# Kernel optimization log

Hardware: AMD Instinct MI355X
Metric: run time of the kernel (lower is better)

Reference implementation:

```python
import jax, jax.numpy as jnp
import numpy as np

SHAPES = ((96, 144), (48, 72), (24, 36), (12, 18))
BS, EMBED = 2, 256
HEADS, LEVELS, POINTS = 8, 4, 4
NEMBED = EMBED // HEADS
LEN_V = sum(h * w for h, w in SHAPES)
LEN_Q = LEN_V  # encoder self-attention: every pixel is a query


def _pos_grid_init():
    # Faithful re-implementation of MultiScaleDeformableAttention.pos_grid_init
    thetas = jnp.arange(HEADS, dtype=jnp.float32) * (2.0 * np.pi / HEADS)
    g = jnp.stack([jnp.cos(thetas), jnp.sin(thetas)], -1)
    g = g / jnp.max(jnp.abs(g), axis=-1, keepdims=True)
    g = jnp.tile(g.reshape(HEADS, 1, 1, 2), (1, LEVELS, POINTS, 1))
    scale = (jnp.arange(POINTS, dtype=jnp.float32) + 1.0)[None, None, :, None]
    return g * scale  # [HEADS, LEVELS, POINTS, 2]


def setup_inputs() -> dict:
    ks = jax.random.split(jax.random.key(0), 7)
    return {
        'query': jax.random.normal(ks[0], (BS, LEN_Q, EMBED), jnp.float32),
        'ref_points': jax.random.uniform(ks[1], (BS, LEN_Q, LEVELS, 2), jnp.float32),
        'value': jax.random.normal(ks[2], (BS, LEN_V, EMBED), jnp.float32),
        'pad_mask': jnp.ones((BS, LEN_V), dtype=bool),
        'value_proj_kernel': jax.random.normal(ks[3], (EMBED, HEADS, NEMBED), jnp.float32) * 0.05,
        'value_proj_bias': jnp.zeros((HEADS, NEMBED), jnp.float32),
        'sampling_offsets_kernel': jax.random.normal(ks[4], (EMBED, HEADS, LEVELS, POINTS, 2), jnp.float32) * 0.01,
        'sampling_offsets_bias': _pos_grid_init(),
        'attn_kernel': jax.random.normal(ks[5], (EMBED, HEADS, LEVELS * POINTS), jnp.float32) * 0.02,
        'attn_bias': jnp.zeros((HEADS, LEVELS * POINTS), jnp.float32),
        'out_kernel': jax.random.normal(ks[6], (HEADS, NEMBED, EMBED), jnp.float32) * 0.05,
        'out_bias': jnp.zeros((EMBED,), jnp.float32),
        'train': 0,
    }


def _bilinear(im, grid, w, h):
    """Batched 2D bilinear interpolation, zero outside the image.

    im:   [B, h*w, e] flattened feature map
    grid: [B, N, 2] normalized coords (pixel centers at (x+0.5)/w, (y+0.5)/h)
    Returns [B, N, e]. Identical math to the original gather-based kernel:
    out-of-bounds corner weights are zeroed, so zero-padding the image by 1
    reproduces the 'empty'-pad + masked-weight scheme exactly.
    """
    B, _, e = im.shape
    imp = jnp.pad(im.reshape(B, h, w, e), ((0, 0), (1, 1), (1, 1), (0, 0)))
    imp = imp.reshape(B, (h + 2) * (w + 2), e)
    x = grid[..., 0] * w - 0.5
    y = grid[..., 1] * h - 0.5
    x0 = jnp.floor(x).astype(jnp.int32)
    y0 = jnp.floor(y).astype(jnp.int32)
    x1 = x0 + 1
    y1 = y0 + 1

    def gather(yy, xx):
        idx = jnp.clip(yy + 1, 0, h + 1) * (w + 2) + jnp.clip(xx + 1, 0, w + 1)
        return jnp.take_along_axis(imp, idx[..., None], axis=1)  # [B, N, e]

    x0f, y0f = x0.astype(x.dtype), y0.astype(y.dtype)
    x1f, y1f = x1.astype(x.dtype), y1.astype(y.dtype)
    inx0 = (x0 >= 0) & (x0 <= w - 1)
    inx1 = (x1 >= 0) & (x1 <= w - 1)
    iny0 = (y0 >= 0) & (y0 <= h - 1)
    iny1 = (y1 >= 0) & (y1 <= h - 1)
    wa = jnp.where(inx0 & iny0, (x1f - x) * (y1f - y), 0.0)
    wb = jnp.where(inx0 & iny1, (x1f - x) * (y - y0f), 0.0)
    wc = jnp.where(inx1 & iny0, (x - x0f) * (y1f - y), 0.0)
    wd = jnp.where(inx1 & iny1, (x - x0f) * (y - y0f), 0.0)
    return (gather(y0, x0) * wa[..., None] + gather(y1, x0) * wb[..., None]
            + gather(y0, x1) * wc[..., None] + gather(y1, x1) * wd[..., None])


def _forward(query, ref_points, value, pad_mask, vpk, vpb, sok, sob, ak, ab, okern, obias):
    bs, len_q, _ = query.shape
    len_v = value.shape[1]
    # value projection + pad masking -> [bs*H, len_v, nembed]
    v = jnp.einsum('bve,ehd->bvhd', value, vpk) + vpb
    v = jnp.where(pad_mask[..., None, None], v, 0)
    v = v.transpose(0, 2, 1, 3).reshape(bs * HEADS, len_v, NEMBED)
    # sampling locations (ref_dim == 2 branch) -> [bs*H, L, P*len_q, 2]
    off = jnp.einsum('bqe,ehlpc->bqhlpc', query, sok) + sob
    offset_norm = jnp.array([[w, h] for h, w in SHAPES], dtype=query.dtype)  # [L, 2]
    loc = ref_points[:, :, None, :, None, :] + off / offset_norm[None, None, None, :, None, :]
    loc = loc.transpose(0, 2, 3, 4, 1, 5).reshape(bs * HEADS, LEVELS, POINTS * len_q, 2)
    # attention weights (softmax over L*P) -> [bs*H, len_q, L*P]
    aw = jnp.einsum('bqe,ehm->bqhm', query, ak) + ab
    aw = jax.nn.softmax(aw, axis=-1)
    aw = aw.transpose(0, 2, 1, 3).reshape(bs * HEADS, len_q, LEVELS * POINTS)
    # per-level bilinear sampling, concatenated level-major over (level, point)
    starts = np.cumsum([0] + [h * w for h, w in SHAPES])
    sampled = []
    for li, (h, w) in enumerate(SHAPES):
        vl = v[:, starts[li]:starts[li + 1], :]
        s = _bilinear(vl, loc[:, li], w, h)  # [bs*H, P*len_q, nembed]
        sampled.append(s.reshape(bs * HEADS, POINTS, len_q, NEMBED))
    sampled = jnp.concatenate(sampled, axis=1)  # [bs*H, L*P, len_q, nembed]
    x = jnp.einsum('blqe,bql->bqe', sampled, aw)
    x = x.reshape(bs, HEADS, len_q, NEMBED)
    # output projection: DenseGeneral over (heads, nembed)
    return jnp.einsum('bhqe,hed->bqd', x, okern) + obias


def reference(query, ref_points, value, pad_mask, value_proj_kernel, value_proj_bias,
              sampling_offsets_kernel, sampling_offsets_bias, attn_kernel, attn_bias,
              out_kernel, out_bias, train):
    del train  # eval mode (no remat); math is identical
    return _forward(query, ref_points, value, pad_mask, value_proj_kernel, value_proj_bias,
                    sampling_offsets_kernel, sampling_offsets_bias, attn_kernel, attn_bias,
                    out_kernel, out_bias)
```

## Files before the change

### kernel.cpp

```cpp
#include <hip/hip_runtime.h>
#include <math.h>

#define LEN 18360
#define M_ROWS (2 * LEN)
#define NTASK (16 * LEN)

typedef unsigned short u16;
typedef __attribute__((ext_vector_type(8))) short bf16x8;
typedef __attribute__((ext_vector_type(4))) float f32x4;

__device__ __forceinline__ u16 f2bf(float f) {
  unsigned u = __float_as_uint(f);
  return (u16)((u + 0x7fffu + ((u >> 16) & 1u)) >> 16);
}
__device__ __forceinline__ void async_cp16(const void* g, void* l) {
  __builtin_amdgcn_global_load_lds(
      (const __attribute__((address_space(1))) unsigned*)g,
      (__attribute__((address_space(3))) unsigned*)l, 16, 0, 0);
}

template <int OUT>
__global__ __launch_bounds__(256) void gemm_mfma_k(
    const u16* __restrict__ A, const u16* __restrict__ Bt,
    const float* __restrict__ bias, void* __restrict__ Cv, int M, int N) {
  __shared__ u16 A_lds[8 * 512];
  __shared__ u16 B_lds[8 * 512];

  const int tid = threadIdx.x;
  const int w = tid >> 6;
  const int lane = tid & 63;
  const int wm = w & 1, wn = w >> 1;
  const int m0 = (int)blockIdx.y << 7;
  const int n0 = (int)blockIdx.x << 7;

  const int mr = lane & 15;
  const int kq = (lane >> 4) * 8;

  f32x4 acc[4][4];
#pragma unroll
  for (int i = 0; i < 4; i++)
#pragma unroll
    for (int j = 0; j < 4; j++) acc[i][j] = (f32x4){0.f, 0.f, 0.f, 0.f};

  for (int k0 = 0; k0 < 256; k0 += 32) {
    __syncthreads();
#pragma unroll
    for (int t = 0; t < 2; t++) {
      const int st = 2 * w + t;
      const int ga = min(m0 + st * 16 + mr, M - 1);
      async_cp16(A + (size_t)ga * 256 + k0 + kq, &A_lds[st * 512]);
      const int gb = n0 + st * 16 + mr;
      async_cp16(Bt + (size_t)gb * 256 + k0 + kq, &B_lds[st * 512]);
    }
    __syncthreads();

    bf16x8 af[4], bf[4];
#pragma unroll
    for (int i = 0; i < 4; i++)
      af[i] = *(const bf16x8*)&A_lds[(wm * 4 + i) * 512 + lane * 8];
#pragma unroll
    for (int j = 0; j < 4; j++)
      bf[j] = *(const bf16x8*)&B_lds[(wn * 4 + j) * 512 + lane * 8];
#pragma unroll
    for (int i = 0; i < 4; i++)
#pragma unroll
      for (int j = 0; j < 4; j++)
        acc[i][j] = __builtin_amdgcn_mfma_f32_16x16x32_bf16(bf[j], af[i],
                                                            acc[i][j], 0, 0, 0);
  }

#pragma unroll
  for (int i = 0; i < 4; i++) {
    const int row = m0 + wm * 64 + i * 16 + mr;
    if (row >= M) continue;
#pragma unroll
    for (int j = 0; j < 4; j++) {
      const int col = n0 + wn * 64 + j * 16 + (lane >> 4) * 4;
      const float4 b4 = *(const float4*)(bias + col);
      float4 o;
      o.x = acc[i][j][0] + b4.x;
      o.y = acc[i][j][1] + b4.y;
      o.z = acc[i][j][2] + b4.z;
      o.w = acc[i][j][3] + b4.w;
      if (OUT == 0) {
        *(float4*)((float*)Cv + (size_t)row * N + col) = o;
      } else if (OUT == 1) {
        const int b = row >= LEN;
        const int lv = row - b * LEN;
        const int h = col >> 5, d = col & 31;
        *(float4*)((float*)Cv + ((size_t)((b * 8 + h) * LEN + lv)) * 32 + d) = o;
      } else {
        uint2 p;
        p.x = (unsigned)f2bf(o.x) | ((unsigned)f2bf(o.y) << 16);
        p.y = (unsigned)f2bf(o.z) | ((unsigned)f2bf(o.w) << 16);
        *(uint2*)((u16*)Cv + (size_t)row * N + col) = p;
      }
    }
  }
}

__global__ __launch_bounds__(256) void cast_qv_k(const float* __restrict__ q,
                                                 const float* __restrict__ v,
                                                 u16* __restrict__ qb,
                                                 u16* __restrict__ vb) {
  const size_t i = ((size_t)blockIdx.x * 256 + threadIdx.x) * 4;
  float4 a = *(const float4*)(q + i);
  uint2 p;
  p.x = (unsigned)f2bf(a.x) | ((unsigned)f2bf(a.y) << 16);
  p.y = (unsigned)f2bf(a.z) | ((unsigned)f2bf(a.w) << 16);
  *(uint2*)&qb[i] = p;
  float4 c = *(const float4*)(v + i);
  p.x = (unsigned)f2bf(c.x) | ((unsigned)f2bf(c.y) << 16);
  p.y = (unsigned)f2bf(c.z) | ((unsigned)f2bf(c.w) << 16);
  *(uint2*)&vb[i] = p;
}

__global__ __launch_bounds__(256) void wcast_k(
    const float* __restrict__ vpk, const float* __restrict__ sok,
    const float* __restrict__ ak, const float* __restrict__ ok,
    u16* __restrict__ vpk_t, u16* __restrict__ sok_t, u16* __restrict__ ak_t,
    u16* __restrict__ ok_t) {
  const int gid = blockIdx.x * 256 + threadIdx.x;
  if (gid < 65536) {
    const int d = gid, n = d >> 8, k = d & 255;
    vpk_t[d] = f2bf(vpk[k * 256 + n]);
  } else if (gid < 131072) {
    const int d = gid - 65536, n = d >> 8, k = d & 255;
    sok_t[d] = f2bf(sok[k * 256 + n]);
  } else if (gid < 163840) {
    const int d = gid - 131072, n = d >> 8, k = d & 255;
    ak_t[d] = f2bf(ak[k * 128 + n]);
  } else {
    const int d = gid - 163840, n = d >> 8, k = d & 255;
    ok_t[d] = f2bf(ok[k * 256 + n]);
  }
}

__global__ __launch_bounds__(256) void sampler_k(
    const float* __restrict__ v,
    const u16* __restrict__ offb,
    const u16* __restrict__ awb,
    const float* __restrict__ refp,
    u16* __restrict__ xb)
{
  __shared__ int2 meta[4][258];
  const int tid = threadIdx.x;

  const int cW[4] = {144, 72, 36, 18};
  const int cH[4] = {96, 48, 24, 12};
  const int cS[4] = {0, 13824, 17280, 18144};

  {
    const int t = tid >> 4;
    const int s = tid & 15;
    const int l = s >> 2;

    const int task = (blockIdx.x << 4) + t;
    const int q = task % LEN;
    const int bh = task / LEN;
    const int h = bh & 7;
    const int b = bh >> 3;
    const size_t qrow = (size_t)(b * LEN + q);

    const float logit =
        __uint_as_float((unsigned)awb[qrow * 128 + h * 16 + s] << 16);
    float mx = logit;
#pragma unroll
    for (int m = 1; m < 16; m <<= 1) mx = fmaxf(mx, __shfl_xor(mx, m, 16));
    const float e = __expf(logit - mx);
    float ssum = e;
#pragma unroll
    for (int m = 1; m < 16; m <<= 1) ssum += __shfl_xor(ssum, m, 16);
    const float wsm = e / ssum;

    const int W = cW[l], H = cH[l], ST = cS[l];
    const float2 rp = ((const float2*)(refp + qrow * 8))[l];
    const unsigned upair = ((const unsigned*)(offb + qrow * 256 + h * 32))[s];
    const float ox = __uint_as_float(upair << 16);
    const float oy = __uint_as_float(upair & 0xffff0000u);
    const float X = rp.x * (float)W + ox - 0.5f;
    const float Y = rp.y * (float)H + oy - 0.5f;
    const float fx = floorf(X), fy = floorf(Y);
    const int x0 = (int)fx, y0 = (int)fy;
    const float dx = X - fx, dy = Y - fy;
    const float ux = 1.f - dx, uy = 1.f - dy;
    const bool bx0 = (unsigned)x0 < (unsigned)W;
    const bool bx1 = (unsigned)(x0 + 1) < (unsigned)W;
    const bool by0 = (unsigned)y0 < (unsigned)H;
    const bool by1 = (unsigned)(y0 + 1) < (unsigned)H;
    const int xc0 = min(max(x0, 0), W - 1);
    const int xc1 = min(max(x0 + 1, 0), W - 1);
    const int yc0 = min(max(y0, 0), H - 1);
    const int yc1 = min(max(y0 + 1, 0), H - 1);
    const float w00 = (bx0 & by0) ? wsm * ux * uy : 0.f;
    const float w10 = (bx1 & by0) ? wsm * dx * uy : 0.f;
    const float w01 = (bx0 & by1) ? wsm * ux * dy : 0.f;
    const float w11 = (bx1 & by1) ? wsm * dx * dy : 0.f;

    meta[0][tid] = make_int2((ST + yc0 * W + xc0) << 7, __float_as_int(w00));
    meta[1][tid] = make_int2((ST + yc0 * W + xc1) << 7, __float_as_int(w10));
    meta[2][tid] = make_int2((ST + yc1 * W + xc0) << 7, __float_as_int(w01));
    meta[3][tid] = make_int2((ST + yc1 * W + xc1) << 7, __float_as_int(w11));
  }
  __syncthreads();

  const int u = tid >> 5;
  const int lane = tid & 31;
  const int c = lane >> 3;
  const int dq = lane & 7;

#pragma unroll
  for (int rep = 0; rep < 2; rep++) {
    const int t = u + rep * 8;
    const int task = (blockIdx.x << 4) + t;
    const int q = task % LEN;
    const int bh = task / LEN;
    const int h = bh & 7;
    const int b = bh >> 3;
    const size_t qrow = (size_t)(b * LEN + q);
    const char* vb = (const char*)v + (size_t)bh * LEN * 128;

    float4 acc = make_float4(0.f, 0.f, 0.f, 0.f);
#pragma unroll
    for (int s = 0; s < 16; s++) {
      const int2 m2 = meta[c][t * 16 + s];
      const float wgt = __int_as_float(m2.y);
      const float4 vv =
          *(const float4*)(vb + (size_t)(unsigned)m2.x + (dq << 4));
      acc.x = fmaf(wgt, vv.x, acc.x);
      acc.y = fmaf(wgt, vv.y, acc.y);
      acc.z = fmaf(wgt, vv.z, acc.z);
      acc.w = fmaf(wgt, vv.w, acc.w);
    }
#pragma unroll
    for (int m = 8; m <= 16; m <<= 1) {
      acc.x += __shfl_xor(acc.x, m, 32);
      acc.y += __shfl_xor(acc.y, m, 32);
      acc.z += __shfl_xor(acc.z, m, 32);
      acc.w += __shfl_xor(acc.w, m, 32);
    }
    if (c == 0) {
      uint2 p;
      p.x = (unsigned)f2bf(acc.x) | ((unsigned)f2bf(acc.y) << 16);
      p.y = (unsigned)f2bf(acc.z) | ((unsigned)f2bf(acc.w) << 16);
      *(uint2*)&xb[qrow * 256 + h * 32 + (dq << 2)] = p;
    }
  }
}

extern "C" void kernel_launch(void* const* d_in, const int* in_sizes, int n_in,
                              void* d_out, int out_size, void* d_ws,
                              size_t ws_size, hipStream_t stream) {
  (void)in_sizes; (void)n_in; (void)out_size; (void)ws_size;

  const float* query = (const float*)d_in[0];
  const float* refp = (const float*)d_in[1];
  const float* value = (const float*)d_in[2];
  const float* vpk = (const float*)d_in[4];
  const float* vpb = (const float*)d_in[5];
  const float* sok = (const float*)d_in[6];
  const float* sob = (const float*)d_in[7];
  const float* ak = (const float*)d_in[8];
  const float* ab = (const float*)d_in[9];
  const float* okern = (const float*)d_in[10];
  const float* obias = (const float*)d_in[11];

  char* ws = (char*)d_ws;
  float* v_ws = (float*)ws;
  char* p = ws + (size_t)M_ROWS * 256 * 4;
  u16* off_b = (u16*)p; p += (size_t)M_ROWS * 256 * 2;
  u16* aw_b = (u16*)p;  p += (size_t)M_ROWS * 128 * 2;
  u16* qbf = (u16*)p;   p += (size_t)M_ROWS * 256 * 2;
  u16* vbf = (u16*)p;   p += (size_t)M_ROWS * 256 * 2;
  u16* vpk_t = (u16*)p; p += 65536 * 2;
  u16* sok_t = (u16*)p; p += 65536 * 2;
  u16* ak_t = (u16*)p;  p += 32768 * 2;
  u16* ok_t = (u16*)p;
  u16* x_b = qbf;

  const dim3 blk(256);
  const int mtiles = (M_ROWS + 127) / 128;

  cast_qv_k<<<dim3(2350080 / 256), blk, 0, stream>>>(query, value, qbf, vbf);
  wcast_k<<<dim3(896), blk, 0, stream>>>(vpk, sok, ak, okern, vpk_t, sok_t,
                                         ak_t, ok_t);
  gemm_mfma_k<1><<<dim3(2, mtiles), blk, 0, stream>>>(vbf, vpk_t, vpb, v_ws,
                                                      M_ROWS, 256);
  gemm_mfma_k<2><<<dim3(2, mtiles), blk, 0, stream>>>(qbf, sok_t, sob, off_b,
                                                      M_ROWS, 256);
  gemm_mfma_k<2><<<dim3(1, mtiles), blk, 0, stream>>>(qbf, ak_t, ab, aw_b,
                                                      M_ROWS, 128);
  sampler_k<<<dim3(NTASK / 16), blk, 0, stream>>>(v_ws, off_b, aw_b, refp,
                                                  x_b);
  gemm_mfma_k<0><<<dim3(2, mtiles), blk, 0, stream>>>(x_b, ok_t, obias,
                                                      (float*)d_out, M_ROWS,
                                                      256);
}
```

Before: 299.3 us.

## Merge projection GEMMs into one launch and store projected values as bf16

After: 275.5 us. 1.09x faster.

```diff
diff --git a/kernel.cpp b/kernel.cpp
--- a/kernel.cpp
+++ b/kernel.cpp
@@ -19,20 +19,34 @@
       (__attribute__((address_space(3))) unsigned*)l, 16, 0, 0);
 }
 
-template <int OUT>
 __global__ __launch_bounds__(256) void gemm_mfma_k(
-    const u16* __restrict__ A, const u16* __restrict__ Bt,
-    const float* __restrict__ bias, void* __restrict__ Cv, int M, int N) {
+    const u16* __restrict__ A0, const u16* __restrict__ Bt0,
+    const float* __restrict__ bias0, void* __restrict__ C0, int N0, int nt0,
+    int mode0, int split, const u16* __restrict__ A1,
+    const u16* __restrict__ Bt1, const float* __restrict__ bias1,
+    void* __restrict__ C1, int N1, int nt1, int mode1) {
   __shared__ u16 A_lds[8 * 512];
   __shared__ u16 B_lds[8 * 512];
+
+  int bid = (int)blockIdx.x;
+  const u16* A;
+  const u16* Bt;
+  const float* bias;
+  void* Cv;
+  int N, nt, mode;
+  if (bid < split) {
+    A = A0; Bt = Bt0; bias = bias0; Cv = C0; N = N0; nt = nt0; mode = mode0;
+  } else {
+    bid -= split;
+    A = A1; Bt = Bt1; bias = bias1; Cv = C1; N = N1; nt = nt1; mode = mode1;
+  }
+  const int n0 = (bid % nt) << 7;
+  const int m0 = (bid / nt) << 7;
 
   const int tid = threadIdx.x;
   const int w = tid >> 6;
   const int lane = tid & 63;
   const int wm = w & 1, wn = w >> 1;
-  const int m0 = (int)blockIdx.y << 7;
-  const int n0 = (int)blockIdx.x << 7;
-
   const int mr = lane & 15;
   const int kq = (lane >> 4) * 8;
 
@@ -47,7 +61,7 @@
 #pragma unroll
     for (int t = 0; t < 2; t++) {
       const int st = 2 * w + t;
-      const int ga = min(m0 + st * 16 + mr, M - 1);
+      const int ga = min(m0 + st * 16 + mr, M_ROWS - 1);
       async_cp16(A + (size_t)ga * 256 + k0 + kq, &A_lds[st * 512]);
       const int gb = n0 + st * 16 + mr;
       async_cp16(Bt + (size_t)gb * 256 + k0 + kq, &B_lds[st * 512]);
@@ -72,7 +86,7 @@
 #pragma unroll
   for (int i = 0; i < 4; i++) {
     const int row = m0 + wm * 64 + i * 16 + mr;
-    if (row >= M) continue;
+    if (row >= M_ROWS) continue;
 #pragma unroll
     for (int j = 0; j < 4; j++) {
       const int col = n0 + wn * 64 + j * 16 + (lane >> 4) * 4;
@@ -82,13 +96,16 @@
       o.y = acc[i][j][1] + b4.y;
       o.z = acc[i][j][2] + b4.z;
       o.w = acc[i][j][3] + b4.w;
-      if (OUT == 0) {
+      if (mode == 0) {
         *(float4*)((float*)Cv + (size_t)row * N + col) = o;
-      } else if (OUT == 1) {
+      } else if (mode == 1) {
         const int b = row >= LEN;
         const int lv = row - b * LEN;
         const int h = col >> 5, d = col & 31;
-        *(float4*)((float*)Cv + ((size_t)((b * 8 + h) * LEN + lv)) * 32 + d) = o;
+        uint2 p;
+        p.x = (unsigned)f2bf(o.x) | ((unsigned)f2bf(o.y) << 16);
+        p.y = (unsigned)f2bf(o.z) | ((unsigned)f2bf(o.w) << 16);
+        *(uint2*)((u16*)Cv + ((size_t)((b * 8 + h) * LEN + lv)) * 32 + d) = p;
       } else {
         uint2 p;
         p.x = (unsigned)f2bf(o.x) | ((unsigned)f2bf(o.y) << 16);
@@ -118,28 +135,31 @@
 __global__ __launch_bounds__(256) void wcast_k(
     const float* __restrict__ vpk, const float* __restrict__ sok,
     const float* __restrict__ ak, const float* __restrict__ ok,
-    u16* __restrict__ vpk_t, u16* __restrict__ sok_t, u16* __restrict__ ak_t,
-    u16* __restrict__ ok_t) {
+    const float* __restrict__ sob, const float* __restrict__ ab,
+    u16* __restrict__ vpk_t, u16* __restrict__ sa_t, u16* __restrict__ ok_t,
+    float* __restrict__ bias_cat) {
   const int gid = blockIdx.x * 256 + threadIdx.x;
   if (gid < 65536) {
     const int d = gid, n = d >> 8, k = d & 255;
     vpk_t[d] = f2bf(vpk[k * 256 + n]);
   } else if (gid < 131072) {
     const int d = gid - 65536, n = d >> 8, k = d & 255;
-    sok_t[d] = f2bf(sok[k * 256 + n]);
+    sa_t[d] = f2bf(sok[k * 256 + n]);
   } else if (gid < 163840) {
     const int d = gid - 131072, n = d >> 8, k = d & 255;
-    ak_t[d] = f2bf(ak[k * 128 + n]);
-  } else {
+    sa_t[65536 + d] = f2bf(ak[k * 128 + n]);
+  } else if (gid < 229376) {
     const int d = gid - 163840, n = d >> 8, k = d & 255;
     ok_t[d] = f2bf(ok[k * 256 + n]);
+  } else if (gid < 229760) {
+    const int d = gid - 229376;
+    bias_cat[d] = (d < 256) ? sob[d] : ab[d - 256];
   }
 }
 
 __global__ __launch_bounds__(256) void sampler_k(
-    const float* __restrict__ v,
-    const u16* __restrict__ offb,
-    const u16* __restrict__ awb,
+    const u16* __restrict__ v,
+    const u16* __restrict__ offaw,
     const float* __restrict__ refp,
     u16* __restrict__ xb)
 {
@@ -161,9 +181,9 @@
     const int h = bh & 7;
     const int b = bh >> 3;
     const size_t qrow = (size_t)(b * LEN + q);
-
-    const float logit =
-        __uint_as_float((unsigned)awb[qrow * 128 + h * 16 + s] << 16);
+    const u16* rowp = offaw + qrow * 384;
+
+    const float logit = __uint_as_float((unsigned)rowp[256 + h * 16 + s] << 16);
     float mx = logit;
 #pragma unroll
     for (int m = 1; m < 16; m <<= 1) mx = fmaxf(mx, __shfl_xor(mx, m, 16));
@@ -175,7 +195,7 @@
 
     const int W = cW[l], H = cH[l], ST = cS[l];
     const float2 rp = ((const float2*)(refp + qrow * 8))[l];
-    const unsigned upair = ((const unsigned*)(offb + qrow * 256 + h * 32))[s];
+    const unsigned upair = ((const unsigned*)(rowp + h * 32))[s];
     const float ox = __uint_as_float(upair << 16);
     const float oy = __uint_as_float(upair & 0xffff0000u);
     const float X = rp.x * (float)W + ox - 0.5f;
@@ -197,10 +217,10 @@
     const float w01 = (bx0 & by1) ? wsm * ux * dy : 0.f;
     const float w11 = (bx1 & by1) ? wsm * dx * dy : 0.f;
 
-    meta[0][tid] = make_int2((ST + yc0 * W + xc0) << 7, __float_as_int(w00));
-    meta[1][tid] = make_int2((ST + yc0 * W + xc1) << 7, __float_as_int(w10));
-    meta[2][tid] = make_int2((ST + yc1 * W + xc0) << 7, __float_as_int(w01));
-    meta[3][tid] = make_int2((ST + yc1 * W + xc1) << 7, __float_as_int(w11));
+    meta[0][tid] = make_int2((ST + yc0 * W + xc0) << 6, __float_as_int(w00));
+    meta[1][tid] = make_int2((ST + yc0 * W + xc1) << 6, __float_as_int(w10));
+    meta[2][tid] = make_int2((ST + yc1 * W + xc0) << 6, __float_as_int(w01));
+    meta[3][tid] = make_int2((ST + yc1 * W + xc1) << 6, __float_as_int(w11));
   }
   __syncthreads();
 
@@ -218,19 +238,18 @@
     const int h = bh & 7;
     const int b = bh >> 3;
     const size_t qrow = (size_t)(b * LEN + q);
-    const char* vb = (const char*)v + (size_t)bh * LEN * 128;
+    const char* vb = (const char*)v + (size_t)bh * LEN * 64;
 
     float4 acc = make_float4(0.f, 0.f, 0.f, 0.f);
 #pragma unroll
     for (int s = 0; s < 16; s++) {
       const int2 m2 = meta[c][t * 16 + s];
       const float wgt = __int_as_float(m2.y);
-      const float4 vv =
-          *(const float4*)(vb + (size_t)(unsigned)m2.x + (dq << 4));
-      acc.x = fmaf(wgt, vv.x, acc.x);
-      acc.y = fmaf(wgt, vv.y, acc.y);
-      acc.z = fmaf(wgt, vv.z, acc.z);
-      acc.w = fmaf(wgt, vv.w, acc.w);
+      const uint2 pv = *(const uint2*)(vb + (size_t)(unsigned)m2.x + (dq << 3));
+      acc.x = fmaf(wgt, __uint_as_float(pv.x << 16), acc.x);
+      acc.y = fmaf(wgt, __uint_as_float(pv.x & 0xffff0000u), acc.y);
+      acc.z = fmaf(wgt, __uint_as_float(pv.y << 16), acc.z);
+      acc.w = fmaf(wgt, __uint_as_float(pv.y & 0xffff0000u), acc.w);
     }
 #pragma unroll
     for (int m = 8; m <= 16; m <<= 1) {
@@ -265,34 +284,28 @@
   const float* okern = (const float*)d_in[10];
   const float* obias = (const float*)d_in[11];
 
-  char* ws = (char*)d_ws;
-  float* v_ws = (float*)ws;
-  char* p = ws + (size_t)M_ROWS * 256 * 4;
-  u16* off_b = (u16*)p; p += (size_t)M_ROWS * 256 * 2;
-  u16* aw_b = (u16*)p;  p += (size_t)M_ROWS * 128 * 2;
-  u16* qbf = (u16*)p;   p += (size_t)M_ROWS * 256 * 2;
-  u16* vbf = (u16*)p;   p += (size_t)M_ROWS * 256 * 2;
-  u16* vpk_t = (u16*)p; p += 65536 * 2;
-  u16* sok_t = (u16*)p; p += 65536 * 2;
-  u16* ak_t = (u16*)p;  p += 32768 * 2;
-  u16* ok_t = (u16*)p;
+  char* p = (char*)d_ws;
+  u16* v_ws = (u16*)p;   p += (size_t)M_ROWS * 256 * 2;
+  u16* offaw = (u16*)p;  p += (size_t)M_ROWS * 384 * 2;
+  u16* qbf = (u16*)p;    p += (size_t)M_ROWS * 256 * 2;
+  u16* vbf = (u16*)p;    p += (size_t)M_ROWS * 256 * 2;
+  u16* vpk_t = (u16*)p;  p += 65536 * 2;
+  u16* sa_t = (u16*)p;   p += 98304 * 2;
+  u16* ok_t = (u16*)p;   p += 65536 * 2;
+  float* bias_cat = (float*)p;
   u16* x_b = qbf;
 
   const dim3 blk(256);
-  const int mtiles = (M_ROWS + 127) / 128;
+  const int mt = (M_ROWS + 127) / 128;
 
   cast_qv_k<<<dim3(2350080 / 256), blk, 0, stream>>>(query, value, qbf, vbf);
-  wcast_k<<<dim3(896), blk, 0, stream>>>(vpk, sok, ak, okern, vpk_t, sok_t,
-                                         ak_t, ok_t);
-  gemm_mfma_k<1><<<dim3(2, mtiles), blk, 0, stream>>>(vbf, vpk_t, vpb, v_ws,
-                                                      M_ROWS, 256);
-  gemm_mfma_k<2><<<dim3(2, mtiles), blk, 0, stream>>>(qbf, sok_t, sob, off_b,
-                                                      M_ROWS, 256);
-  gemm_mfma_k<2><<<dim3(1, mtiles), blk, 0, stream>>>(qbf, ak_t, ab, aw_b,
-                                                      M_ROWS, 128);
-  sampler_k<<<dim3(NTASK / 16), blk, 0, stream>>>(v_ws, off_b, aw_b, refp,
-                                                  x_b);
-  gemm_mfma_k<0><<<dim3(2, mtiles), blk, 0, stream>>>(x_b, ok_t, obias,
-                                                      (float*)d_out, M_ROWS,
-                                                      256);
-}
+  wcast_k<<<dim3(898), blk, 0, stream>>>(vpk, sok, ak, okern, sob, ab, vpk_t,
+                                         sa_t, ok_t, bias_cat);
+  gemm_mfma_k<<<dim3(2 * mt + 3 * mt), blk, 0, stream>>>(
+      vbf, vpk_t, vpb, v_ws, 256, 2, 1, 2 * mt,
+      qbf, sa_t, bias_cat, offaw, 384, 3, 2);
+  sampler_k<<<dim3(NTASK / 16), blk, 0, stream>>>(v_ws, offaw, refp, x_b);
+  gemm_mfma_k<<<dim3(2 * mt), blk, 0, stream>>>(
+      x_b, ok_t, obias, (float*)d_out, 256, 2, 0, 2 * mt,
+      x_b, ok_t, obias, (float*)d_out, 256, 2, 0);
+}
```
